# Kernel optimization log

Hardware: AMD Instinct MI355X
Metric: run time of the kernel (lower is better)

Reference implementation:

```python
import jax, jax.numpy as jnp
import numpy as np

N_RES = 3      # n_resblock (weights SHARED across layers, matching [block]*n in torch)
N_E = 1024     # n_embeddings
E_DIM = 64     # dim_embeddings
P = 4
BETA = 0.25
B = 16384      # batch rows
IN = 128       # input_size
DENC = 512     # dim_encoder
DOUT = E_DIM * P  # dim_encoder_out = 256


def setup_inputs() -> dict:
    key = jax.random.key(0)
    ks = jax.random.split(key, 16)
    def w(k, o, i):
        return jax.random.normal(k, (o, i), jnp.float32) * 0.02
    return {
        "x": jax.random.normal(ks[0], (B, IN), jnp.float32),
        "a": jax.random.normal(ks[1], (B, IN), jnp.float32),
        "scale": 1.0 + 0.1 * jax.random.normal(ks[2], (IN,), jnp.float32),
        "shift": 0.01 * jax.random.normal(ks[3], (IN,), jnp.float32),
        "enc_win_w": w(ks[4], DENC, IN), "enc_win_b": jnp.zeros((DENC,), jnp.float32),
        "enc_ain_w": w(ks[5], DENC, IN), "enc_ain_b": jnp.zeros((DENC,), jnp.float32),
        "enc_wres_w": w(ks[6], DENC, DENC), "enc_wres_b": jnp.zeros((DENC,), jnp.float32),
        "enc_wres_g": jnp.ones((DENC,), jnp.float32), "enc_wres_be": jnp.zeros((DENC,), jnp.float32),
        "enc_ares_w": w(ks[7], DENC, DENC), "enc_ares_b": jnp.zeros((DENC,), jnp.float32),
        "enc_ares_g": jnp.ones((DENC,), jnp.float32), "enc_ares_be": jnp.zeros((DENC,), jnp.float32),
        "enc_out_w": w(ks[8], DOUT, DENC), "enc_out_b": jnp.zeros((DOUT,), jnp.float32),
        "dec1_w": w(ks[9], DENC, DOUT), "dec1_b": jnp.zeros((DENC,), jnp.float32),
        "dec_res_w": w(ks[10], DENC, DENC), "dec_res_b": jnp.zeros((DENC,), jnp.float32),
        "dec_res_g": jnp.ones((DENC,), jnp.float32), "dec_res_be": jnp.zeros((DENC,), jnp.float32),
        "dec2_w": w(ks[11], IN, DENC), "dec2_b": jnp.zeros((IN,), jnp.float32),
        "codebook": jax.random.uniform(ks[12], (N_E, E_DIM), jnp.float32, -1.0 / N_E, 1.0 / N_E),
    }


def _ln(h, g, b, eps=1e-5):
    m = jnp.mean(h, axis=-1, keepdims=True)
    v = jnp.var(h, axis=-1, keepdims=True)
    return (h - m) * jax.lax.rsqrt(v + eps) * g + b


def _resblock(x, w, b, g, be):
    # Linear -> LayerNorm -> ReLU, residual add
    h = x @ w.T + b
    return x + jax.nn.relu(_ln(h, g, be))


def reference(x, a, scale, shift,
              enc_win_w, enc_win_b, enc_ain_w, enc_ain_b,
              enc_wres_w, enc_wres_b, enc_wres_g, enc_wres_be,
              enc_ares_w, enc_ares_b, enc_ares_g, enc_ares_be,
              enc_out_w, enc_out_b,
              dec1_w, dec1_b,
              dec_res_w, dec_res_b, dec_res_g, dec_res_be,
              dec2_w, dec2_b, codebook):
    sg = jax.lax.stop_gradient
    # --- input normalization ---
    xs = (x - shift) / scale
    # --- Encoder (weight path modulated by activation-magnitude path) ---
    av = a @ enc_ain_w.T + enc_ain_b
    h = xs @ enc_win_w.T + enc_win_b
    for _ in range(N_RES):  # shared weights per stack, interleaved mul
        av = _resblock(av, enc_ares_w, enc_ares_b, enc_ares_g, enc_ares_be)
        h = _resblock(h, enc_wres_w, enc_wres_b, enc_wres_g, enc_wres_be) * av
    z_e = h @ enc_out_w.T + enc_out_b  # (B, P*E_DIM)
    # --- Vector quantization (cdist + argmin + gather) ---
    zf = z_e.reshape(-1, E_DIM)  # (B*P, E_DIM)
    d = (jnp.sum(zf * zf, axis=1, keepdims=True)
         + jnp.sum(codebook * codebook, axis=1)
         - 2.0 * zf @ codebook.T)  # (B*P, N_E)
    idx = jnp.argmin(d, axis=1)  # (B*P,)
    z_q = codebook[idx].reshape(z_e.shape)
    loss = (jnp.mean((sg(z_q) - z_e) ** 2)
            + BETA * jnp.mean((z_q - sg(z_e)) ** 2))
    z_q_st = z_e + sg(z_q - z_e)  # straight-through
    counts = jnp.zeros((N_E,), jnp.float32).at[idx].add(1.0)
    e_mean = counts / zf.shape[0]
    perplexity = jnp.exp(-jnp.sum(e_mean * jnp.log(e_mean + 1e-10)))
    # --- Decoder ---
    hd = z_q_st @ dec1_w.T + dec1_b
    for _ in range(N_RES):
        hd = _resblock(hd, dec_res_w, dec_res_b, dec_res_g, dec_res_be)
    x_hat = hd @ dec2_w.T + dec2_b
    x_hat = scale * x_hat + shift
    return (loss, x_hat, perplexity, z_q_st, idx)
```

## Files before the change

### kernel.cpp

```cpp
#include <hip/hip_runtime.h>
#include <hip/hip_bf16.h>
#include <math.h>

static constexpr int BROWS = 16384;
static constexpr int IND   = 128;
static constexpr int DE    = 512;
static constexpr int DOUTD = 256;
static constexpr int ED    = 64;
static constexpr int NE    = 1024;

static constexpr size_t O_XHAT = 1;
static constexpr size_t O_PERP = 2097153;
static constexpr size_t O_ZQ   = 2097154;
static constexpr size_t O_IDX  = 6291458;

typedef __attribute__((ext_vector_type(8))) short short8v;
typedef __attribute__((ext_vector_type(4))) float f32x4;
typedef __attribute__((ext_vector_type(4))) unsigned short ushort4v;
typedef __attribute__((ext_vector_type(8))) unsigned short ushort8v;

__device__ inline float wave_sum(float v) {
#pragma unroll
    for (int o = 32; o >= 1; o >>= 1) v += __shfl_xor(v, o, 64);
    return v;
}

__device__ inline unsigned short f2bf(float f) {
    unsigned u = __float_as_uint(f);
    return (unsigned short)((u + 0x7FFFu + ((u >> 16) & 1u)) >> 16);
}
__device__ inline float bf2f(unsigned short b) {
    return __uint_as_float(((unsigned)b) << 16);
}
struct Split3 { unsigned short b0, b1, b2; };
__device__ inline Split3 split3(float v) {
    Split3 s;
    s.b0 = f2bf(v);  float r  = v - bf2f(s.b0);
    s.b1 = f2bf(r);  float r2 = r - bf2f(s.b1);
    s.b2 = f2bf(r2);
    return s;
}

template<int K>
__global__ __launch_bounds__(256)
void gemm8_k(const unsigned short* __restrict__ A0, const unsigned short* __restrict__ A1,
             const unsigned short* __restrict__ A2,
             const unsigned short* __restrict__ W0, const unsigned short* __restrict__ W1,
             const unsigned short* __restrict__ W2,
             const float* __restrict__ bias, float* __restrict__ C, int N)
{
    __shared__ short As[3][128 * 40];
    __shared__ short Ws[3][128 * 40];
    const int t = threadIdx.x;
    const int bm = blockIdx.y << 7, bn = blockIdx.x << 7;
    const int lane = t & 63, wid = t >> 6;
    const int wm = (wid >> 1) << 6, wn = (wid & 1) << 6;
    const int lr = lane & 15, lg = lane >> 4;
    const unsigned short* Ap[3] = {A0, A1, A2};
    const unsigned short* Wp[3] = {W0, W1, W2};
    f32x4 acc[4][4] = {};
    for (int k0 = 0; k0 < K; k0 += 32) {
#pragma unroll
        for (int p = 0; p < 3; ++p) {
#pragma unroll
            for (int s = 0; s < 2; ++s) {
                int c = t + (s << 8);
                int row = c >> 2, kc = (c & 3) << 3;
                *(short8v*)&As[p][row * 40 + kc] =
                    *(const short8v*)(Ap[p] + (size_t)(bm + row) * K + k0 + kc);
                *(short8v*)&Ws[p][row * 40 + kc] =
                    *(const short8v*)(Wp[p] + (size_t)(bn + row) * K + k0 + kc);
            }
        }
        __syncthreads();
        short8v bfr[3][4];
#pragma unroll
        for (int p = 0; p < 3; ++p)
#pragma unroll
            for (int nj = 0; nj < 4; ++nj)
                bfr[p][nj] = *(const short8v*)&Ws[p][(wn + nj * 16 + lr) * 40 + lg * 8];
#pragma unroll
        for (int mi = 0; mi < 4; ++mi) {
            short8v a0 = *(const short8v*)&As[0][(wm + mi * 16 + lr) * 40 + lg * 8];
            short8v a1 = *(const short8v*)&As[1][(wm + mi * 16 + lr) * 40 + lg * 8];
            short8v a2 = *(const short8v*)&As[2][(wm + mi * 16 + lr) * 40 + lg * 8];
#pragma unroll
            for (int nj = 0; nj < 4; ++nj) {
                f32x4 c = acc[mi][nj];
                c = __builtin_amdgcn_mfma_f32_16x16x32_bf16(a2, bfr[1][nj], c, 0, 0, 0);
                c = __builtin_amdgcn_mfma_f32_16x16x32_bf16(a1, bfr[2][nj], c, 0, 0, 0);
                c = __builtin_amdgcn_mfma_f32_16x16x32_bf16(a1, bfr[1][nj], c, 0, 0, 0);
                c = __builtin_amdgcn_mfma_f32_16x16x32_bf16(a2, bfr[0][nj], c, 0, 0, 0);
                c = __builtin_amdgcn_mfma_f32_16x16x32_bf16(a0, bfr[2][nj], c, 0, 0, 0);
                c = __builtin_amdgcn_mfma_f32_16x16x32_bf16(a1, bfr[0][nj], c, 0, 0, 0);
                c = __builtin_amdgcn_mfma_f32_16x16x32_bf16(a0, bfr[1][nj], c, 0, 0, 0);
                c = __builtin_amdgcn_mfma_f32_16x16x32_bf16(a0, bfr[0][nj], c, 0, 0, 0);
                acc[mi][nj] = c;
            }
        }
        __syncthreads();
    }
#pragma unroll
    for (int mi = 0; mi < 4; ++mi)
#pragma unroll
        for (int nj = 0; nj < 4; ++nj)
#pragma unroll
            for (int r = 0; r < 4; ++r) {
                int m = bm + wm + mi * 16 + lg * 4 + r;
                int n = bn + wn + nj * 16 + lr;
                C[(size_t)m * N + n] = acc[mi][nj][r] + bias[n];
            }
}

template<int K, int EPI>
__global__ __launch_bounds__(256)
void gemmbf_k(const short* __restrict__ A, const short* __restrict__ W,
              const float* __restrict__ bias, float* __restrict__ C, int N,
              unsigned short* __restrict__ Cb,
              const float* __restrict__ escale, const float* __restrict__ eshift)
{
    __shared__ short As[128 * 40];
    __shared__ short Ws[128 * 40];
    const int t = threadIdx.x;
    const int bm = blockIdx.y << 7, bn = blockIdx.x << 7;
    const int lane = t & 63, wid = t >> 6;
    const int wm = (wid >> 1) << 6, wn = (wid & 1) << 6;
    const int lr = lane & 15, lg = lane >> 4;
    f32x4 acc[4][4] = {};
    for (int k0 = 0; k0 < K; k0 += 32) {
#pragma unroll
        for (int s = 0; s < 2; ++s) {
            int c = t + (s << 8);
            int row = c >> 2, kc = (c & 3) << 3;
            *(short8v*)&As[row * 40 + kc] = *(const short8v*)(A + (size_t)(bm + row) * K + k0 + kc);
            *(short8v*)&Ws[row * 40 + kc] = *(const short8v*)(W + (size_t)(bn + row) * K + k0 + kc);
        }
        __syncthreads();
        short8v af[4], bf[4];
#pragma unroll
        for (int mi = 0; mi < 4; ++mi) af[mi] = *(const short8v*)&As[(wm + mi * 16 + lr) * 40 + lg * 8];
#pragma unroll
        for (int nj = 0; nj < 4; ++nj) bf[nj] = *(const short8v*)&Ws[(wn + nj * 16 + lr) * 40 + lg * 8];
#pragma unroll
        for (int mi = 0; mi < 4; ++mi)
#pragma unroll
            for (int nj = 0; nj < 4; ++nj)
                acc[mi][nj] = __builtin_amdgcn_mfma_f32_16x16x32_bf16(af[mi], bf[nj], acc[mi][nj], 0, 0, 0);
        __syncthreads();
    }
#pragma unroll
    for (int mi = 0; mi < 4; ++mi)
#pragma unroll
        for (int nj = 0; nj < 4; ++nj)
#pragma unroll
            for (int r = 0; r < 4; ++r) {
                int m = bm + wm + mi * 16 + lg * 4 + r;
                int n = bn + wn + nj * 16 + lr;
                float v = acc[mi][nj][r] + bias[n];
                if (EPI == 2) v = escale[n] * v + eshift[n];
                C[(size_t)m * N + n] = v;
                if (EPI == 1) Cb[(size_t)m * N + n] = f2bf(v);
            }
}

__global__ __launch_bounds__(256)
void prep_split_k(const float* __restrict__ x, const float* __restrict__ scale,
                  const float* __restrict__ shift,
                  unsigned short* __restrict__ d0, unsigned short* __restrict__ d1,
                  unsigned short* __restrict__ d2)
{
    int g = blockIdx.x * 256 + threadIdx.x;
    float4 v = *(const float4*)(x + (size_t)g * 4);
    int col = (g * 4) & (IND - 1);
    float vals[4] = {v.x, v.y, v.z, v.w};
    ushort4v o0, o1, o2;
#pragma unroll
    for (int i = 0; i < 4; ++i) {
        float xs = (vals[i] - shift[col + i]) / scale[col + i];
        Split3 s = split3(xs);
        o0[i] = s.b0; o1[i] = s.b1; o2[i] = s.b2;
    }
    *(ushort4v*)(d0 + (size_t)g * 4) = o0;
    *(ushort4v*)(d1 + (size_t)g * 4) = o1;
    *(ushort4v*)(d2 + (size_t)g * 4) = o2;
}

__global__ __launch_bounds__(256)
void split3_k(const float* __restrict__ src,
              unsigned short* __restrict__ d0, unsigned short* __restrict__ d1,
              unsigned short* __restrict__ d2, int n4)
{
    int g = blockIdx.x * 256 + threadIdx.x;
    if (g >= n4) return;
    float4 v = *(const float4*)(src + (size_t)g * 4);
    float vals[4] = {v.x, v.y, v.z, v.w};
    ushort4v o0, o1, o2;
#pragma unroll
    for (int i = 0; i < 4; ++i) {
        Split3 s = split3(vals[i]);
        o0[i] = s.b0; o1[i] = s.b1; o2[i] = s.b2;
    }
    *(ushort4v*)(d0 + (size_t)g * 4) = o0;
    *(ushort4v*)(d1 + (size_t)g * 4) = o1;
    *(ushort4v*)(d2 + (size_t)g * 4) = o2;
}

__global__ __launch_bounds__(256)
void cvt_k(const float* __restrict__ src, unsigned short* __restrict__ dst, int n)
{
    int g = blockIdx.x * 256 + threadIdx.x;
    if (g < n) dst[g] = f2bf(src[g]);
}

__global__ __launch_bounds__(256)
void ln_av_k(const float* __restrict__ T,
             unsigned short* __restrict__ s0, unsigned short* __restrict__ s1,
             unsigned short* __restrict__ s2,
             const float* __restrict__ g, const float* __restrict__ be)
{
    const int lane = threadIdx.x & 63;
    const int row  = (blockIdx.x << 2) + (threadIdx.x >> 6);
    const int col  = lane << 3;
    const size_t base = (size_t)row * DE + col;
    float t[8];
    { float4 p0 = *(const float4*)(T + base); float4 p1 = *(const float4*)(T + base + 4);
      t[0]=p0.x; t[1]=p0.y; t[2]=p0.z; t[3]=p0.w; t[4]=p1.x; t[5]=p1.y; t[6]=p1.z; t[7]=p1.w; }
    float s = 0.f;
#pragma unroll
    for (int i = 0; i < 8; ++i) s += t[i];
    s = wave_sum(s);
    float mean = s * (1.0f / 512.0f);
    float vs = 0.f;
#pragma unroll
    for (int i = 0; i < 8; ++i) { float d = t[i] - mean; vs += d * d; }
    vs = wave_sum(vs);
    float rstd = 1.0f / sqrtf(vs * (1.0f / 512.0f) + 1e-5f);
    ushort8v b0 = *(const ushort8v*)(s0 + base);
    ushort8v b1 = *(const ushort8v*)(s1 + base);
    ushort8v b2 = *(const ushort8v*)(s2 + base);
    ushort8v o0, o1, o2;
#pragma unroll
    for (int i = 0; i < 8; ++i) {
        float avv = bf2f(b0[i]) + bf2f(b1[i]) + bf2f(b2[i]);
        float lnv = (t[i] - mean) * rstd * g[col + i] + be[col + i];
        float avn = avv + fmaxf(lnv, 0.0f);
        Split3 sp = split3(avn);
        o0[i] = sp.b0; o1[i] = sp.b1; o2[i] = sp.b2;
    }
    *(ushort8v*)(s0 + base) = o0;
    *(ushort8v*)(s1 + base) = o1;
    *(ushort8v*)(s2 + base) = o2;
}

__global__ __launch_bounds__(256)
void ln_h_k(const float* __restrict__ T,
            unsigned short* __restrict__ s0, unsigned short* __restrict__ s1,
            unsigned short* __restrict__ s2,
            const unsigned short* __restrict__ a0, const unsigned short* __restrict__ a1,
            const unsigned short* __restrict__ a2,
            const float* __restrict__ g, const float* __restrict__ be)
{
    const int lane = threadIdx.x & 63;
    const int row  = (blockIdx.x << 2) + (threadIdx.x >> 6);
    const int col  = lane << 3;
    const size_t base = (size_t)row * DE + col;
    float t[8];
    { float4 p0 = *(const float4*)(T + base); float4 p1 = *(const float4*)(T + base + 4);
      t[0]=p0.x; t[1]=p0.y; t[2]=p0.z; t[3]=p0.w; t[4]=p1.x; t[5]=p1.y; t[6]=p1.z; t[7]=p1.w; }
    float s = 0.f;
#pragma unroll
    for (int i = 0; i < 8; ++i) s += t[i];
    s = wave_sum(s);
    float mean = s * (1.0f / 512.0f);
    float vs = 0.f;
#pragma unroll
    for (int i = 0; i < 8; ++i) { float d = t[i] - mean; vs += d * d; }
    vs = wave_sum(vs);
    float rstd = 1.0f / sqrtf(vs * (1.0f / 512.0f) + 1e-5f);
    ushort8v h0 = *(const ushort8v*)(s0 + base);
    ushort8v h1 = *(const ushort8v*)(s1 + base);
    ushort8v h2 = *(const ushort8v*)(s2 + base);
    ushort8v v0 = *(const ushort8v*)(a0 + base);
    ushort8v v1 = *(const ushort8v*)(a1 + base);
    ushort8v v2 = *(const ushort8v*)(a2 + base);
    ushort8v o0, o1, o2;
#pragma unroll
    for (int i = 0; i < 8; ++i) {
        float hv  = bf2f(h0[i]) + bf2f(h1[i]) + bf2f(h2[i]);
        float avn = bf2f(v0[i]) + bf2f(v1[i]) + bf2f(v2[i]);
        float lnv = (t[i] - mean) * rstd * g[col + i] + be[col + i];
        float hn  = (hv + fmaxf(lnv, 0.0f)) * avn;
        Split3 sp = split3(hn);
        o0[i] = sp.b0; o1[i] = sp.b1; o2[i] = sp.b2;
    }
    *(ushort8v*)(s0 + base) = o0;
    *(ushort8v*)(s1 + base) = o1;
    *(ushort8v*)(s2 + base) = o2;
}

__global__ __launch_bounds__(256)
void ln_dec_k(const float* __restrict__ t_, float* __restrict__ h,
              const float* __restrict__ g, const float* __restrict__ be,
              unsigned short* __restrict__ hb)
{
    const int lane = threadIdx.x & 63;
    const int row  = (blockIdx.x << 2) + (threadIdx.x >> 6);
    const int col  = lane << 3;
    const size_t base = (size_t)row * DE + col;
    float t[8];
    { float4 p0 = *(const float4*)(t_ + base); float4 p1 = *(const float4*)(t_ + base + 4);
      t[0]=p0.x; t[1]=p0.y; t[2]=p0.z; t[3]=p0.w; t[4]=p1.x; t[5]=p1.y; t[6]=p1.z; t[7]=p1.w; }
    float s = 0.f;
#pragma unroll
    for (int i = 0; i < 8; ++i) s += t[i];
    s = wave_sum(s);
    float mean = s * (1.0f / 512.0f);
    float vs = 0.f;
#pragma unroll
    for (int i = 0; i < 8; ++i) { float d = t[i] - mean; vs += d * d; }
    vs = wave_sum(vs);
    float rstd = 1.0f / sqrtf(vs * (1.0f / 512.0f) + 1e-5f);
    float4 p0 = *(const float4*)(h + base); float4 p1 = *(const float4*)(h + base + 4);
    float hv[8] = {p0.x,p0.y,p0.z,p0.w,p1.x,p1.y,p1.z,p1.w};
    float hn[8];
    ushort8v ob;
#pragma unroll
    for (int i = 0; i < 8; ++i) {
        float lnv = (t[i] - mean) * rstd * g[col + i] + be[col + i];
        hn[i] = hv[i] + fmaxf(lnv, 0.0f);
        ob[i] = f2bf(hn[i]);
    }
    float4 o0 = {hn[0],hn[1],hn[2],hn[3]}, o1 = {hn[4],hn[5],hn[6],hn[7]};
    *(float4*)(h + base) = o0; *(float4*)(h + base + 4) = o1;
    *(ushort8v*)(hb + base) = ob;
}

__global__ __launch_bounds__(256)
void c2_k(const float* __restrict__ cb, float* __restrict__ c2)
{
    int j = blockIdx.x * 256 + threadIdx.x;
    if (j < NE) {
        float s = 0.f;
        const float* p = cb + (size_t)j * ED;
#pragma unroll
        for (int d = 0; d < ED; ++d) s = fmaf(p[d], p[d], s);
        c2[j] = s;
    }
}

__global__ __launch_bounds__(256)
void vq_k(const float* __restrict__ ze, const float* __restrict__ cb, const float* __restrict__ c2,
          float* __restrict__ idx_dst, float* __restrict__ zst_dst,
          unsigned short* __restrict__ zb,
          int* __restrict__ counts, float* __restrict__ partials)
{
    __shared__ float zs[64 * 68];
    __shared__ float cbs[64 * 132];
    __shared__ float z2s[64];
    __shared__ float c2s[128];
    __shared__ int   bidxs[64];
    __shared__ float red[4];
    const int t = threadIdx.x;
    const int tx = t & 15, ty = t >> 4;
    const size_t row0 = (size_t)blockIdx.x * 64;

#pragma unroll
    for (int s = 0; s < 4; ++s) {
        int c = t + (s << 8);
        int row = c >> 4, dc = (c & 15) << 2;
        float4 v = *(const float4*)(ze + (row0 + row) * 64 + dc);
        *(float4*)&zs[row * 68 + dc] = v;
    }
    __syncthreads();
    if (t < 64) {
        float z2 = 0.f;
#pragma unroll 8
        for (int d = 0; d < 64; ++d) { float zv = zs[t * 68 + d]; z2 = fmaf(zv, zv, z2); }
        z2s[t] = z2;
    }

    float best[4] = {INFINITY, INFINITY, INFINITY, INFINITY};
    int   bid[4]  = {0, 0, 0, 0};
    for (int t0 = 0; t0 < NE; t0 += 128) {
        __syncthreads();
#pragma unroll
        for (int s = 0; s < 8; ++s) {
            int c = t + (s << 8);
            int code = c >> 4, dc = (c & 15) << 2;
            float4 v = *(const float4*)(cb + (size_t)(t0 + code) * 64 + dc);
            cbs[(dc + 0) * 132 + code] = v.x; cbs[(dc + 1) * 132 + code] = v.y;
            cbs[(dc + 2) * 132 + code] = v.z; cbs[(dc + 3) * 132 + code] = v.w;
        }
        if (t < 128) c2s[t] = c2[t0 + t];
        __syncthreads();
        float acc[4][8] = {};
#pragma unroll 8
        for (int kk = 0; kk < 64; ++kk) {
            float a[4];
#pragma unroll
            for (int j = 0; j < 4; ++j) a[j] = zs[(4 * ty + j) * 68 + kk];
            float4 b0 = *(const float4*)&cbs[kk * 132 + (tx << 2)];
            float4 b1 = *(const float4*)&cbs[kk * 132 + 64 + (tx << 2)];
            float bv_[8] = {b0.x, b0.y, b0.z, b0.w, b1.x, b1.y, b1.z, b1.w};
#pragma unroll
            for (int r = 0; r < 4; ++r)
#pragma unroll
                for (int j = 0; j < 8; ++j)
                    acc[r][j] = fmaf(a[r], bv_[j], acc[r][j]);
        }
#pragma unroll
        for (int r = 0; r < 4; ++r) {
            float z2v = z2s[(ty << 2) + r];
#pragma unroll
            for (int j = 0; j < 8; ++j) {
                int cloc = (j < 4) ? ((tx << 2) + j) : (64 + (tx << 2) + (j - 4));
                float term = __fadd_rn(z2v, c2s[cloc]);
                float dist = __fsub_rn(term, __fmul_rn(2.0f, acc[r][j]));
                if (dist < best[r]) { best[r] = dist; bid[r] = t0 + cloc; }
            }
        }
    }
    __syncthreads();
    float* rbd = cbs;
    int*   rbi = (int*)(cbs + 1024);
#pragma unroll
    for (int r = 0; r < 4; ++r) {
        rbd[((ty << 2) + r) * 16 + tx] = best[r];
        rbi[((ty << 2) + r) * 16 + tx] = bid[r];
    }
    __syncthreads();
    if (t < 64) {
        float bd = INFINITY; int bi = 0;
#pragma unroll
        for (int q = 0; q < 16; ++q) {
            float d = rbd[t * 16 + q]; int i = rbi[t * 16 + q];
            if (d < bd || (d == bd && i < bi)) { bd = d; bi = i; }
        }
        bidxs[t] = bi;
        idx_dst[row0 + t] = (float)bi;
        atomicAdd(&counts[bi], 1);
    }
    __syncthreads();
    const int row = t >> 2, cq = t & 3;
    const int bi = bidxs[row];
    float lsum = 0.f;
#pragma unroll
    for (int dd = 0; dd < 16; dd += 4) {
        int d0 = (cq << 4) + dd;
        float4 q4 = *(const float4*)(cb + (size_t)bi * 64 + d0);
        float qv[4] = {q4.x, q4.y, q4.z, q4.w};
        float zst[4];
#pragma unroll
        for (int i = 0; i < 4; ++i) {
            float zv = zs[row * 68 + d0 + i];
            float df = qv[i] - zv;
            lsum = fmaf(df, df, lsum);
            zst[i] = __fadd_rn(zv, __fsub_rn(qv[i], zv));
            zb[(row0 + row) * 64 + d0 + i] = f2bf(zst[i]);
        }
        float2 o0 = {zst[0], zst[1]}, o1 = {zst[2], zst[3]};
        *(float2*)(zst_dst + (row0 + row) * 64 + d0) = o0;
        *(float2*)(zst_dst + (row0 + row) * 64 + d0 + 2) = o1;
    }
    lsum = wave_sum(lsum);
    if ((t & 63) == 0) red[t >> 6] = lsum;
    __syncthreads();
    if (t == 0) partials[blockIdx.x] = ((red[0] + red[1]) + red[2]) + red[3];
}

__global__ __launch_bounds__(256)
void fin_k(const float* __restrict__ partials, const int* __restrict__ counts,
           float* __restrict__ loss_out, float* __restrict__ perp_out)
{
    __shared__ float red[4];
    __shared__ float red2[4];
    const int tid = threadIdx.x;
    float v = 0.f;
    for (int c = tid; c < 1024; c += 256) v += partials[c];
    float s = wave_sum(v);
    if ((tid & 63) == 0) red[tid >> 6] = s;
    float ep = 0.f;
    for (int c = tid; c < NE; c += 256) {
        float e = (float)counts[c] * (1.0f / 65536.0f);
        ep += e * logf(e + 1e-10f);
    }
    ep = wave_sum(ep);
    if ((tid & 63) == 0) red2[tid >> 6] = ep;
    __syncthreads();
    if (tid == 0) {
        float S = ((red[0] + red[1]) + red[2]) + red[3];
        float E = ((red2[0] + red2[1]) + red2[2]) + red2[3];
        loss_out[0] = 1.25f * (S * (1.0f / 4194304.0f));
        perp_out[0] = expf(-E);
    }
}

extern "C" void kernel_launch(void* const* d_in, const int* in_sizes, int n_in,
                              void* d_out, int out_size, void* d_ws, size_t ws_size,
                              hipStream_t stream)
{
    const float* x       = (const float*)d_in[0];
    const float* a       = (const float*)d_in[1];
    const float* scale   = (const float*)d_in[2];
    const float* shift   = (const float*)d_in[3];
    const float* win_w   = (const float*)d_in[4];
    const float* win_b   = (const float*)d_in[5];
    const float* ain_w   = (const float*)d_in[6];
    const float* ain_b   = (const float*)d_in[7];
    const float* wres_w  = (const float*)d_in[8];
    const float* wres_b  = (const float*)d_in[9];
    const float* wres_g  = (const float*)d_in[10];
    const float* wres_be = (const float*)d_in[11];
    const float* ares_w  = (const float*)d_in[12];
    const float* ares_b  = (const float*)d_in[13];
    const float* ares_g  = (const float*)d_in[14];
    const float* ares_be = (const float*)d_in[15];
    const float* out_w   = (const float*)d_in[16];
    const float* out_b   = (const float*)d_in[17];
    const float* dec1_w  = (const float*)d_in[18];
    const float* dec1_b  = (const float*)d_in[19];
    const float* dres_w  = (const float*)d_in[20];
    const float* dres_b  = (const float*)d_in[21];
    const float* dres_g  = (const float*)d_in[22];
    const float* dres_be = (const float*)d_in[23];
    const float* dec2_w  = (const float*)d_in[24];
    const float* dec2_b  = (const float*)d_in[25];
    const float* cb      = (const float*)d_in[26];

    float* ws = (float*)d_ws;
    unsigned short* u = (unsigned short*)d_ws;
    unsigned short* avS0 = u;
    unsigned short* avS1 = u + 8388608;
    unsigned short* avS2 = u + 16777216;
    unsigned short* hS0  = u + 25165824;
    unsigned short* hS1  = u + 33554432;
    unsigned short* hS2  = u + 41943040;
    float* T  = ws + 25165824;
    float* ZE = T;
    unsigned short* aS0 = u,               *aS1 = u + 2097152,  *aS2 = u + 4194304;
    unsigned short* xsS0 = u + 25165824,   *xsS1 = u + 27262976, *xsS2 = u + 29360128;
    unsigned short* ZB  = u;
    unsigned short* w1b = u + 4194304;
    unsigned short* wrb = u + 4325376;
    unsigned short* w2b = u + 4587520;
    float* t_dec = ws + 4194304;
    float* hd    = ws + 12582912;
    unsigned short* Hb = (unsigned short*)(ws + 29360128);
    unsigned short* wsb = u + 67108864;
    unsigned short* ainS0 = wsb,            *ainS1 = wsb + 65536,  *ainS2 = wsb + 131072;
    unsigned short* winS0 = wsb + 196608,   *winS1 = wsb + 262144, *winS2 = wsb + 327680;
    unsigned short* areS0 = wsb + 393216,   *areS1 = wsb + 655360, *areS2 = wsb + 917504;
    unsigned short* wreS0 = wsb + 1179648,  *wreS1 = wsb + 1441792,*wreS2 = wsb + 1703936;
    unsigned short* outS0 = wsb + 1966080,  *outS1 = wsb + 2097152,*outS2 = wsb + 2228224;
    float* c2v      = ws + 34800000;
    int*   counts   = (int*)(ws + 34801024);
    float* partials = ws + 34802048;

    float* dout = (float*)d_out;

    prep_split_k<<<2048, 256, 0, stream>>>(x, scale, shift, xsS0, xsS1, xsS2);
    split3_k<<<2048, 256, 0, stream>>>(a, aS0, aS1, aS2, 524288);
    split3_k<<<64,  256, 0, stream>>>(ain_w, ainS0, ainS1, ainS2, 16384);
    split3_k<<<64,  256, 0, stream>>>(win_w, winS0, winS1, winS2, 16384);
    split3_k<<<256, 256, 0, stream>>>(ares_w, areS0, areS1, areS2, 65536);
    split3_k<<<256, 256, 0, stream>>>(wres_w, wreS0, wreS1, wreS2, 65536);
    split3_k<<<128, 256, 0, stream>>>(out_w, outS0, outS1, outS2, 32768);
    gemm8_k<128><<<dim3(4, 128), 256, 0, stream>>>(aS0, aS1, aS2, ainS0, ainS1, ainS2, ain_b, T, DE);
    split3_k<<<8192, 256, 0, stream>>>(T, avS0, avS1, avS2, 2097152);
    gemm8_k<128><<<dim3(4, 128), 256, 0, stream>>>(xsS0, xsS1, xsS2, winS0, winS1, winS2, win_b, T, DE);
    split3_k<<<8192, 256, 0, stream>>>(T, hS0, hS1, hS2, 2097152);
    for (int r = 0; r < 3; ++r) {
        gemm8_k<512><<<dim3(4, 128), 256, 0, stream>>>(avS0, avS1, avS2, areS0, areS1, areS2, ares_b, T, DE);
        ln_av_k<<<4096, 256, 0, stream>>>(T, avS0, avS1, avS2, ares_g, ares_be);
        gemm8_k<512><<<dim3(4, 128), 256, 0, stream>>>(hS0, hS1, hS2, wreS0, wreS1, wreS2, wres_b, T, DE);
        ln_h_k<<<4096, 256, 0, stream>>>(T, hS0, hS1, hS2, avS0, avS1, avS2, wres_g, wres_be);
    }
    gemm8_k<512><<<dim3(2, 128), 256, 0, stream>>>(hS0, hS1, hS2, outS0, outS1, outS2, out_b, ZE, DOUTD);
    c2_k<<<NE / 256, 256, 0, stream>>>(cb, c2v);
    (void)hipMemsetAsync(counts, 0, NE * sizeof(int), stream);
    vq_k<<<1024, 256, 0, stream>>>(ZE, cb, c2v, dout + O_IDX, dout + O_ZQ, ZB, counts, partials);
    fin_k<<<1, 256, 0, stream>>>(partials, counts, dout, dout + O_PERP);
    cvt_k<<<512,  256, 0, stream>>>(dec1_w, w1b, DE * DOUTD);
    cvt_k<<<1024, 256, 0, stream>>>(dres_w, wrb, DE * DE);
    cvt_k<<<256,  256, 0, stream>>>(dec2_w, w2b, IND * DE);
    gemmbf_k<256, 1><<<dim3(DE / 128, BROWS / 128), 256, 0, stream>>>(
        (const short*)ZB, (const short*)w1b, dec1_b, hd, DE, Hb, nullptr, nullptr);
    for (int r = 0; r < 3; ++r) {
        gemmbf_k<512, 0><<<dim3(DE / 128, BROWS / 128), 256, 0, stream>>>(
            (const short*)Hb, (const short*)wrb, dres_b, t_dec, DE, nullptr, nullptr, nullptr);
        ln_dec_k<<<4096, 256, 0, stream>>>(t_dec, hd, dres_g, dres_be, Hb);
    }
    gemmbf_k<512, 2><<<dim3(IND / 128, BROWS / 128), 256, 0, stream>>>(
        (const short*)Hb, (const short*)w2b, dec2_b, dout + O_XHAT, IND, nullptr, scale, shift);
}
```

Before: 947.8 us.

## Fuse prep kernels, pair input GEMMs with split epilogue, stream codebook from global

```diff
diff --git a/kernel.cpp b/kernel.cpp
--- a/kernel.cpp
+++ b/kernel.cpp
@@ -41,16 +41,16 @@
     return s;
 }
 
-template<int K>
-__global__ __launch_bounds__(256)
-void gemm8_k(const unsigned short* __restrict__ A0, const unsigned short* __restrict__ A1,
-             const unsigned short* __restrict__ A2,
-             const unsigned short* __restrict__ W0, const unsigned short* __restrict__ W1,
-             const unsigned short* __restrict__ W2,
-             const float* __restrict__ bias, float* __restrict__ C, int N)
-{
-    __shared__ short As[3][128 * 40];
-    __shared__ short Ws[3][128 * 40];
+template<int K, int EPI>
+__device__ inline void gemm8_body(const unsigned short* __restrict__ A0, const unsigned short* __restrict__ A1,
+                                  const unsigned short* __restrict__ A2,
+                                  const unsigned short* __restrict__ W0, const unsigned short* __restrict__ W1,
+                                  const unsigned short* __restrict__ W2,
+                                  const float* __restrict__ bias, float* __restrict__ Cf,
+                                  unsigned short* __restrict__ S0, unsigned short* __restrict__ S1,
+                                  unsigned short* __restrict__ S2, int N,
+                                  short (*As)[128 * 40], short (*Ws)[128 * 40])
+{
     const int t = threadIdx.x;
     const int bm = blockIdx.y << 7, bn = blockIdx.x << 7;
     const int lane = t & 63, wid = t >> 6;
@@ -108,8 +108,42 @@
             for (int r = 0; r < 4; ++r) {
                 int m = bm + wm + mi * 16 + lg * 4 + r;
                 int n = bn + wn + nj * 16 + lr;
-                C[(size_t)m * N + n] = acc[mi][nj][r] + bias[n];
+                float v = acc[mi][nj][r] + bias[n];
+                if (EPI == 0) {
+                    Cf[(size_t)m * N + n] = v;
+                } else {
+                    Split3 sp = split3(v);
+                    S0[(size_t)m * N + n] = sp.b0;
+                    S1[(size_t)m * N + n] = sp.b1;
+                    S2[(size_t)m * N + n] = sp.b2;
+                }
             }
+}
+
+template<int K>
+__global__ __launch_bounds__(256)
+void gemm8_k(const unsigned short* __restrict__ A0, const unsigned short* __restrict__ A1,
+             const unsigned short* __restrict__ A2,
+             const unsigned short* __restrict__ W0, const unsigned short* __restrict__ W1,
+             const unsigned short* __restrict__ W2,
+             const float* __restrict__ bias, float* __restrict__ C, int N)
+{
+    __shared__ short As[3][128 * 40];
+    __shared__ short Ws[3][128 * 40];
+    gemm8_body<K, 0>(A0, A1, A2, W0, W1, W2, bias, C, nullptr, nullptr, nullptr, N, As, Ws);
+}
+
+struct G8S { const unsigned short *A0, *A1, *A2, *W0, *W1, *W2; const float* bias;
+             unsigned short *S0, *S1, *S2; };
+
+__global__ __launch_bounds__(256)
+void gemm8pair_k(G8S ga, G8S gb, int N)
+{
+    __shared__ short As[3][128 * 40];
+    __shared__ short Ws[3][128 * 40];
+    const G8S& g = (blockIdx.z == 0) ? ga : gb;
+    gemm8_body<128, 1>(g.A0, g.A1, g.A2, g.W0, g.W1, g.W2, g.bias, nullptr,
+                       g.S0, g.S1, g.S2, N, As, Ws);
 }
 
 template<int K, int EPI>
@@ -164,35 +198,60 @@
 }
 
 __global__ __launch_bounds__(256)
-void prep_split_k(const float* __restrict__ x, const float* __restrict__ scale,
-                  const float* __restrict__ shift,
-                  unsigned short* __restrict__ d0, unsigned short* __restrict__ d1,
-                  unsigned short* __restrict__ d2)
-{
-    int g = blockIdx.x * 256 + threadIdx.x;
-    float4 v = *(const float4*)(x + (size_t)g * 4);
-    int col = (g * 4) & (IND - 1);
-    float vals[4] = {v.x, v.y, v.z, v.w};
-    ushort4v o0, o1, o2;
-#pragma unroll
-    for (int i = 0; i < 4; ++i) {
-        float xs = (vals[i] - shift[col + i]) / scale[col + i];
-        Split3 s = split3(xs);
-        o0[i] = s.b0; o1[i] = s.b1; o2[i] = s.b2;
-    }
-    *(ushort4v*)(d0 + (size_t)g * 4) = o0;
-    *(ushort4v*)(d1 + (size_t)g * 4) = o1;
-    *(ushort4v*)(d2 + (size_t)g * 4) = o2;
-}
-
-__global__ __launch_bounds__(256)
-void split3_k(const float* __restrict__ src,
-              unsigned short* __restrict__ d0, unsigned short* __restrict__ d1,
-              unsigned short* __restrict__ d2, int n4)
-{
-    int g = blockIdx.x * 256 + threadIdx.x;
-    if (g >= n4) return;
-    float4 v = *(const float4*)(src + (size_t)g * 4);
+void prep2_k(const float* __restrict__ x, const float* __restrict__ scale,
+             const float* __restrict__ shift,
+             unsigned short* __restrict__ x0, unsigned short* __restrict__ x1,
+             unsigned short* __restrict__ x2,
+             const float* __restrict__ a,
+             unsigned short* __restrict__ a0, unsigned short* __restrict__ a1,
+             unsigned short* __restrict__ a2)
+{
+    if (blockIdx.x < 2048) {
+        int g = blockIdx.x * 256 + threadIdx.x;
+        float4 v = *(const float4*)(x + (size_t)g * 4);
+        int col = (g * 4) & (IND - 1);
+        float vals[4] = {v.x, v.y, v.z, v.w};
+        ushort4v o0, o1, o2;
+#pragma unroll
+        for (int i = 0; i < 4; ++i) {
+            float xs = (vals[i] - shift[col + i]) / scale[col + i];
+            Split3 s = split3(xs);
+            o0[i] = s.b0; o1[i] = s.b1; o2[i] = s.b2;
+        }
+        *(ushort4v*)(x0 + (size_t)g * 4) = o0;
+        *(ushort4v*)(x1 + (size_t)g * 4) = o1;
+        *(ushort4v*)(x2 + (size_t)g * 4) = o2;
+    } else {
+        int g = (blockIdx.x - 2048) * 256 + threadIdx.x;
+        float4 v = *(const float4*)(a + (size_t)g * 4);
+        float vals[4] = {v.x, v.y, v.z, v.w};
+        ushort4v o0, o1, o2;
+#pragma unroll
+        for (int i = 0; i < 4; ++i) {
+            Split3 s = split3(vals[i]);
+            o0[i] = s.b0; o1[i] = s.b1; o2[i] = s.b2;
+        }
+        *(ushort4v*)(a0 + (size_t)g * 4) = o0;
+        *(ushort4v*)(a1 + (size_t)g * 4) = o1;
+        *(ushort4v*)(a2 + (size_t)g * 4) = o2;
+    }
+}
+
+__global__ __launch_bounds__(256)
+void wsplit_k(const float* __restrict__ ain_w, const float* __restrict__ win_w,
+              const float* __restrict__ ares_w, const float* __restrict__ wres_w,
+              const float* __restrict__ out_w,
+              unsigned short* __restrict__ wsb)
+{
+    int g4 = blockIdx.x * 256 + threadIdx.x;
+    const float* src; unsigned short *d0, *d1, *d2; int base;
+    if (g4 < 16384)       { src = ain_w;  d0 = wsb;           d1 = wsb + 65536;   d2 = wsb + 131072;  base = 0; }
+    else if (g4 < 32768)  { src = win_w;  d0 = wsb + 196608;  d1 = wsb + 262144;  d2 = wsb + 327680;  base = 16384; }
+    else if (g4 < 98304)  { src = ares_w; d0 = wsb + 393216;  d1 = wsb + 655360;  d2 = wsb + 917504;  base = 32768; }
+    else if (g4 < 163840) { src = wres_w; d0 = wsb + 1179648; d1 = wsb + 1441792; d2 = wsb + 1703936; base = 98304; }
+    else                  { src = out_w;  d0 = wsb + 1966080; d1 = wsb + 2097152; d2 = wsb + 2228224; base = 163840; }
+    int l4 = g4 - base;
+    float4 v = *(const float4*)(src + (size_t)l4 * 4);
     float vals[4] = {v.x, v.y, v.z, v.w};
     ushort4v o0, o1, o2;
 #pragma unroll
@@ -200,16 +259,21 @@
         Split3 s = split3(vals[i]);
         o0[i] = s.b0; o1[i] = s.b1; o2[i] = s.b2;
     }
-    *(ushort4v*)(d0 + (size_t)g * 4) = o0;
-    *(ushort4v*)(d1 + (size_t)g * 4) = o1;
-    *(ushort4v*)(d2 + (size_t)g * 4) = o2;
-}
-
-__global__ __launch_bounds__(256)
-void cvt_k(const float* __restrict__ src, unsigned short* __restrict__ dst, int n)
+    *(ushort4v*)(d0 + (size_t)l4 * 4) = o0;
+    *(ushort4v*)(d1 + (size_t)l4 * 4) = o1;
+    *(ushort4v*)(d2 + (size_t)l4 * 4) = o2;
+}
+
+__global__ __launch_bounds__(256)
+void cvt3_k(const float* __restrict__ dec1_w, const float* __restrict__ dres_w,
+            const float* __restrict__ dec2_w,
+            unsigned short* __restrict__ w1b, unsigned short* __restrict__ wrb,
+            unsigned short* __restrict__ w2b)
 {
     int g = blockIdx.x * 256 + threadIdx.x;
-    if (g < n) dst[g] = f2bf(src[g]);
+    if (g < 131072)       w1b[g] = f2bf(dec1_w[g]);
+    else if (g < 393216)  wrb[g - 131072] = f2bf(dres_w[g - 131072]);
+    else if (g < 458752)  w2b[g - 393216] = f2bf(dec2_w[g - 393216]);
 }
 
 __global__ __launch_bounds__(256)
@@ -336,7 +400,7 @@
 }
 
 __global__ __launch_bounds__(256)
-void c2_k(const float* __restrict__ cb, float* __restrict__ c2)
+void c2z_k(const float* __restrict__ cb, float* __restrict__ c2, int* __restrict__ counts)
 {
     int j = blockIdx.x * 256 + threadIdx.x;
     if (j < NE) {
@@ -345,6 +409,7 @@
 #pragma unroll
         for (int d = 0; d < ED; ++d) s = fmaf(p[d], p[d], s);
         c2[j] = s;
+        counts[j] = 0;
     }
 }
 
@@ -355,9 +420,9 @@
           int* __restrict__ counts, float* __restrict__ partials)
 {
     __shared__ float zs[64 * 68];
-    __shared__ float cbs[64 * 132];
     __shared__ float z2s[64];
-    __shared__ float c2s[128];
+    __shared__ float rbd[64 * 16];
+    __shared__ int   rbi[64 * 16];
     __shared__ int   bidxs[64];
     __shared__ float red[4];
     const int t = threadIdx.x;
@@ -378,35 +443,31 @@
         for (int d = 0; d < 64; ++d) { float zv = zs[t * 68 + d]; z2 = fmaf(zv, zv, z2); }
         z2s[t] = z2;
     }
+    __syncthreads();
 
     float best[4] = {INFINITY, INFINITY, INFINITY, INFINITY};
     int   bid[4]  = {0, 0, 0, 0};
     for (int t0 = 0; t0 < NE; t0 += 128) {
-        __syncthreads();
-#pragma unroll
-        for (int s = 0; s < 8; ++s) {
-            int c = t + (s << 8);
-            int code = c >> 4, dc = (c & 15) << 2;
-            float4 v = *(const float4*)(cb + (size_t)(t0 + code) * 64 + dc);
-            cbs[(dc + 0) * 132 + code] = v.x; cbs[(dc + 1) * 132 + code] = v.y;
-            cbs[(dc + 2) * 132 + code] = v.z; cbs[(dc + 3) * 132 + code] = v.w;
-        }
-        if (t < 128) c2s[t] = c2[t0 + t];
-        __syncthreads();
         float acc[4][8] = {};
-#pragma unroll 8
-        for (int kk = 0; kk < 64; ++kk) {
-            float a[4];
-#pragma unroll
-            for (int j = 0; j < 4; ++j) a[j] = zs[(4 * ty + j) * 68 + kk];
-            float4 b0 = *(const float4*)&cbs[kk * 132 + (tx << 2)];
-            float4 b1 = *(const float4*)&cbs[kk * 132 + 64 + (tx << 2)];
-            float bv_[8] = {b0.x, b0.y, b0.z, b0.w, b1.x, b1.y, b1.z, b1.w};
-#pragma unroll
-            for (int r = 0; r < 4; ++r)
-#pragma unroll
-                for (int j = 0; j < 8; ++j)
-                    acc[r][j] = fmaf(a[r], bv_[j], acc[r][j]);
+#pragma unroll 4
+        for (int kk0 = 0; kk0 < 64; kk0 += 4) {
+            float4 a4[4];
+#pragma unroll
+            for (int r = 0; r < 4; ++r) a4[r] = *(const float4*)&zs[(4 * ty + r) * 68 + kk0];
+#pragma unroll
+            for (int j = 0; j < 8; ++j) {
+                int cloc = (j < 4) ? ((tx << 2) + j) : (64 + (tx << 2) + (j - 4));
+                float4 b4 = *(const float4*)(cb + (size_t)(t0 + cloc) * 64 + kk0);
+#pragma unroll
+                for (int r = 0; r < 4; ++r) {
+                    float acv = acc[r][j];
+                    acv = fmaf(a4[r].x, b4.x, acv);
+                    acv = fmaf(a4[r].y, b4.y, acv);
+                    acv = fmaf(a4[r].z, b4.z, acv);
+                    acv = fmaf(a4[r].w, b4.w, acv);
+                    acc[r][j] = acv;
+                }
+            }
         }
 #pragma unroll
         for (int r = 0; r < 4; ++r) {
@@ -414,15 +475,12 @@
 #pragma unroll
             for (int j = 0; j < 8; ++j) {
                 int cloc = (j < 4) ? ((tx << 2) + j) : (64 + (tx << 2) + (j - 4));
-                float term = __fadd_rn(z2v, c2s[cloc]);
+                float term = __fadd_rn(z2v, c2[t0 + cloc]);
                 float dist = __fsub_rn(term, __fmul_rn(2.0f, acc[r][j]));
                 if (dist < best[r]) { best[r] = dist; bid[r] = t0 + cloc; }
             }
         }
     }
-    __syncthreads();
-    float* rbd = cbs;
-    int*   rbi = (int*)(cbs + 1024);
 #pragma unroll
     for (int r = 0; r < 4; ++r) {
         rbd[((ty << 2) + r) * 16 + tx] = best[r];
@@ -537,8 +595,8 @@
     unsigned short* hS2  = u + 41943040;
     float* T  = ws + 25165824;
     float* ZE = T;
-    unsigned short* aS0 = u,               *aS1 = u + 2097152,  *aS2 = u + 4194304;
-    unsigned short* xsS0 = u + 25165824,   *xsS1 = u + 27262976, *xsS2 = u + 29360128;
+    unsigned short* aS0  = u + 50331648, *aS1  = u + 52428800, *aS2  = u + 54525952;
+    unsigned short* xsS0 = u + 56623104, *xsS1 = u + 58720256, *xsS2 = u + 60817408;
     unsigned short* ZB  = u;
     unsigned short* w1b = u + 4194304;
     unsigned short* wrb = u + 4325376;
@@ -558,17 +616,13 @@
 
     float* dout = (float*)d_out;
 
-    prep_split_k<<<2048, 256, 0, stream>>>(x, scale, shift, xsS0, xsS1, xsS2);
-    split3_k<<<2048, 256, 0, stream>>>(a, aS0, aS1, aS2, 524288);
-    split3_k<<<64,  256, 0, stream>>>(ain_w, ainS0, ainS1, ainS2, 16384);
-    split3_k<<<64,  256, 0, stream>>>(win_w, winS0, winS1, winS2, 16384);
-    split3_k<<<256, 256, 0, stream>>>(ares_w, areS0, areS1, areS2, 65536);
-    split3_k<<<256, 256, 0, stream>>>(wres_w, wreS0, wreS1, wreS2, 65536);
-    split3_k<<<128, 256, 0, stream>>>(out_w, outS0, outS1, outS2, 32768);
-    gemm8_k<128><<<dim3(4, 128), 256, 0, stream>>>(aS0, aS1, aS2, ainS0, ainS1, ainS2, ain_b, T, DE);
-    split3_k<<<8192, 256, 0, stream>>>(T, avS0, avS1, avS2, 2097152);
-    gemm8_k<128><<<dim3(4, 128), 256, 0, stream>>>(xsS0, xsS1, xsS2, winS0, winS1, winS2, win_b, T, DE);
-    split3_k<<<8192, 256, 0, stream>>>(T, hS0, hS1, hS2, 2097152);
+    wsplit_k<<<768, 256, 0, stream>>>(ain_w, win_w, ares_w, wres_w, out_w, wsb);
+    prep2_k<<<4096, 256, 0, stream>>>(x, scale, shift, xsS0, xsS1, xsS2, a, aS0, aS1, aS2);
+    {
+        G8S ga = {aS0, aS1, aS2, ainS0, ainS1, ainS2, ain_b, avS0, avS1, avS2};
+        G8S gb = {xsS0, xsS1, xsS2, winS0, winS1, winS2, win_b, hS0, hS1, hS2};
+        gemm8pair_k<<<dim3(4, 128, 2), 256, 0, stream>>>(ga, gb, DE);
+    }
     for (int r = 0; r < 3; ++r) {
         gemm8_k<512><<<dim3(4, 128), 256, 0, stream>>>(avS0, avS1, avS2, areS0, areS1, areS2, ares_b, T, DE);
         ln_av_k<<<4096, 256, 0, stream>>>(T, avS0, avS1, avS2, ares_g, ares_be);
@@ -576,13 +630,10 @@
         ln_h_k<<<4096, 256, 0, stream>>>(T, hS0, hS1, hS2, avS0, avS1, avS2, wres_g, wres_be);
     }
     gemm8_k<512><<<dim3(2, 128), 256, 0, stream>>>(hS0, hS1, hS2, outS0, outS1, outS2, out_b, ZE, DOUTD);
-    c2_k<<<NE / 256, 256, 0, stream>>>(cb, c2v);
-    (void)hipMemsetAsync(counts, 0, NE * sizeof(int), stream);
+    c2z_k<<<4, 256, 0, stream>>>(cb, c2v, counts);
     vq_k<<<1024, 256, 0, stream>>>(ZE, cb, c2v, dout + O_IDX, dout + O_ZQ, ZB, counts, partials);
     fin_k<<<1, 256, 0, stream>>>(partials, counts, dout, dout + O_PERP);
-    cvt_k<<<512,  256, 0, stream>>>(dec1_w, w1b, DE * DOUTD);
-    cvt_k<<<1024, 256, 0, stream>>>(dres_w, wrb, DE * DE);
-    cvt_k<<<256,  256, 0, stream>>>(dec2_w, w2b, IND * DE);
+    cvt3_k<<<1792, 256, 0, stream>>>(dec1_w, dres_w, dec2_w, w1b, wrb, w2b);
     gemmbf_k<256, 1><<<dim3(DE / 128, BROWS / 128), 256, 0, stream>>>(
         (const short*)ZB, (const short*)w1b, dec1_b, hd, DE, Hb, nullptr, nullptr);
     for (int r = 0; r < 3; ++r) {
```

New measurement: 1.377 ms. 1.45x slower.
